# Performance work log

Measured on AMD Instinct MI355X. Metric: run time of the kernel, lower is better.

Reference implementation:

```python
import jax, jax.numpy as jnp
import numpy as np

# --- Config (Kimi/DeepSeek-style fine-grained MoE) ---
T = 4096        # num tokens
H = 1024        # hidden_size
I = 512         # moe_intermediate_size
E = 64          # num_experts
K = 8           # num_experts_per_token (top_k)
NG = 8          # num_expert_group
TKG = 4         # topk_group
NSH = 2         # num_shared_experts
IS = I * NSH    # shared-expert intermediate size
ROUTED_SCALE = 2.5


def setup_inputs() -> dict:
    key = jax.random.key(0)
    ks = jax.random.split(key, 7)
    s = 0.02
    return {
        "hidden_states": jax.random.normal(ks[0], (T, H), jnp.float32),
        "gate_w": jax.random.normal(ks[1], (E, H), jnp.float32) * s,          # router
        "e_bias": jax.random.normal(ks[2], (E,), jnp.float32) * 0.01,          # e_score_correction_bias
        "w1": jax.random.normal(ks[3], (E, H, 2 * I), jnp.float32) * s,       # per-expert gate_up
        "w2": jax.random.normal(ks[4], (E, I, H), jnp.float32) * s,           # per-expert down
        "sw_gu": jax.random.normal(ks[5], (H, 2 * IS), jnp.float32) * s,      # shared gate_up
        "sw_d": jax.random.normal(ks[6], (IS, H), jnp.float32) * s,           # shared down
    }


def _silu_and_mul(gu):
    d = gu.shape[-1] // 2
    return jax.nn.silu(gu[..., :d]) * gu[..., d:]


def _grouped_topk(scores, e_bias):
    """DeepSeek-V3/Kimi grouped top-k with sigmoid scoring + score-correction bias."""
    Tn = scores.shape[0]
    sfc = scores + e_bias[None, :]                       # scores_for_choice [T, E]
    # group score = sum of top-2 corrected scores inside each group
    grp = sfc.reshape(Tn, NG, E // NG)
    group_scores = jax.lax.top_k(grp, 2)[0].sum(-1)      # [T, NG]
    gidx = jax.lax.top_k(group_scores, TKG)[1]           # [T, TKG]
    gmask = jnp.zeros((Tn, NG), sfc.dtype).at[jnp.arange(Tn)[:, None], gidx].set(1.0)
    smask = jnp.repeat(gmask, E // NG, axis=1) > 0       # [T, E] bool
    tmp = jnp.where(smask, sfc, 0.0)                     # masked_fill(~mask, 0.0) as in vLLM
    topk_ids = jax.lax.top_k(tmp, K)[1]                  # [T, K]
    topk_w = jnp.take_along_axis(scores, topk_ids, axis=1)
    topk_w = topk_w / topk_w.sum(-1, keepdims=True)      # renormalize
    return topk_w, topk_ids


def _forward(x, gate_w, e_bias, w1, w2, sw_gu, sw_d):
    Tn, Hn = x.shape
    # shared experts (KimiMLP)
    shared = _silu_and_mul(x @ sw_gu) @ sw_d             # [T, H]
    # router
    logits = x @ gate_w.T                                # [T, E]
    scores = jax.nn.sigmoid(logits)
    topk_w, topk_ids = _grouped_topk(scores, e_bias)
    # dispatch: sort the T*K assignments by expert id -> grouped GEMM
    flat_ids = topk_ids.reshape(-1)                      # [T*K]
    order = jnp.argsort(flat_ids)                        # [T*K]
    tok = order // K                                     # token index of each sorted assignment
    xs = x[tok]                                          # [T*K, H] gathered tokens
    gsizes = jnp.bincount(flat_ids, length=E).astype(jnp.int32)
    gu = jax.lax.ragged_dot(xs, w1, gsizes)              # [T*K, 2I] grouped GEMM
    h = _silu_and_mul(gu)                                # [T*K, I]
    ys = jax.lax.ragged_dot(h, w2, gsizes)               # [T*K, H]
    # combine: scale by routing weight, scatter-add back to tokens
    flat_w = topk_w.reshape(-1)[order]                   # [T*K]
    routed = jnp.zeros((Tn, Hn), x.dtype).at[tok].add(ys * flat_w[:, None])
    return routed * ROUTED_SCALE + shared


def reference(hidden_states, gate_w, e_bias, w1, w2, sw_gu, sw_d):
    return _forward(hidden_states, gate_w, e_bias, w1, w2, sw_gu, sw_d)
```

## Files before the change

### kernel.cpp

```cpp
#include <hip/hip_runtime.h>
#include <cstdint>
#include <cstddef>

#define TT   4096
#define HH   1024
#define II   512
#define EE   64
#define KT   8
#define ISZ  1024
#define TKA  32768
#define MAXT 320

typedef __bf16 bf16x8 __attribute__((ext_vector_type(8)));
typedef float  f32x4  __attribute__((ext_vector_type(4)));
typedef unsigned short us8v __attribute__((ext_vector_type(8)));

__device__ __forceinline__ unsigned short f2bf(float f) {
  unsigned u = __float_as_uint(f);
  u += 0x7fffu + ((u >> 16) & 1u);
  return (unsigned short)(u >> 16);
}

#define GLDS(gp, lp) __builtin_amdgcn_global_load_lds( \
    (const __attribute__((address_space(1))) void*)(gp), \
    (__attribute__((address_space(3))) void*)(lp), 16, 0, 0)


__global__ __launch_bounds__(256) void k_transpose(const float* __restrict__ in,
                                                   unsigned short* __restrict__ out,
                                                   int R, int C) {
  __shared__ float tile[64][65];
  long b = blockIdx.z;
  int r0 = blockIdx.x * 64, c0 = blockIdx.y * 64;
  const float* ip = in + b * (long)R * C;
  unsigned short* op = out + b * (long)R * C;
  int tc = threadIdx.x & 63, tr = threadIdx.x >> 6;
#pragma unroll
  for (int rr = 0; rr < 64; rr += 4)
    tile[tr + rr][tc] = ip[(long)(r0 + tr + rr) * C + (c0 + tc)];
  __syncthreads();
#pragma unroll
  for (int rr = 0; rr < 64; rr += 4)
    op[(long)(c0 + tr + rr) * R + (r0 + tc)] = f2bf(tile[tc][tr + rr]);
}

__global__ __launch_bounds__(256) void k_cvt(const float* __restrict__ in,
                                             unsigned short* __restrict__ out) {
  int i = blockIdx.x * 256 + threadIdx.x;
  float4 v = ((const float4*)in)[i];
  ushort4 o;
  o.x = f2bf(v.x); o.y = f2bf(v.y); o.z = f2bf(v.z); o.w = f2bf(v.w);
  ((ushort4*)out)[i] = o;
}

__global__ __launch_bounds__(256) void k_router(const float* __restrict__ x,
    const float* __restrict__ gw, const float* __restrict__ eb,
    int* __restrict__ topk_ids, float* __restrict__ topk_w, int* __restrict__ counts)
{
  __shared__ float xrow[HH];
  __shared__ float sc[EE];
  int t = blockIdx.x;
  int tid = threadIdx.x;
  for (int i = tid; i < HH; i += 256) xrow[i] = x[(long)t * HH + i];
  __syncthreads();
  int e = tid >> 2, q = tid & 3;
  const float* w = gw + (long)e * HH;
  double acc = 0.0, acc2 = 0.0;
  for (int i = q * 8; i < HH; i += 32) {
    float4 wa = *(const float4*)(w + i);
    float4 wb = *(const float4*)(w + i + 4);
    acc  += (double)wa.x * (double)xrow[i]
          + (double)wa.y * (double)xrow[i + 1]
          + (double)wa.z * (double)xrow[i + 2]
          + (double)wa.w * (double)xrow[i + 3];
    acc2 += (double)wb.x * (double)xrow[i + 4]
          + (double)wb.y * (double)xrow[i + 5]
          + (double)wb.z * (double)xrow[i + 6]
          + (double)wb.w * (double)xrow[i + 7];
  }
  acc += acc2;
  acc += __shfl_down(acc, 2);
  acc += __shfl_down(acc, 1);
  if (q == 0) sc[e] = (float)(1.0 / (1.0 + exp(-acc)));
  __syncthreads();
  if (tid < 64) {
    int lane = tid;
    float s = sc[lane];
    float sfc = s + eb[lane];
    float m1 = sfc, m2 = -1e30f;
#pragma unroll
    for (int d = 1; d < 8; d <<= 1) {
      float o1 = __shfl_xor(m1, d);
      float o2 = __shfl_xor(m2, d);
      float hi = fmaxf(m1, o1);
      float lo = fminf(m1, o1);
      m2 = fmaxf(lo, fmaxf(m2, o2));
      m1 = hi;
    }
    float gs = m1 + m2;
    int g = lane >> 3;
    int grank = 0;
#pragma unroll
    for (int j = 0; j < 8; j++) {
      float gj = __shfl(gs, j * 8);
      if (gj > gs || (gj == gs && j < g)) grank++;
    }
    bool gsel = grank < 4;
    float mv = gsel ? sfc : 0.0f;
    int rank = 0;
    for (int j = 0; j < 64; j++) {
      float vj = __shfl(mv, j);
      if (vj > mv || (vj == mv && j < lane)) rank++;
    }
    bool sel = rank < KT;
    float ssum = sel ? s : 0.0f;
#pragma unroll
    for (int d = 1; d < 64; d <<= 1) ssum += __shfl_xor(ssum, d);
    unsigned long long bal = __ballot(sel);
    if (sel) {
      int pos = __popcll(bal & ((1ull << lane) - 1ull));
      topk_ids[(long)t * KT + pos] = lane;
      topk_w[(long)t * KT + pos] = s / ssum;
      atomicAdd(&counts[lane], 1);
    }
  }
}

__global__ void k_offsets(const int* __restrict__ counts, int* __restrict__ offsets,
                          int* __restrict__ cursor, int* __restrict__ tile_e,
                          int* __restrict__ tile_r0)
{
  int lane = threadIdx.x;
  int c = counts[lane];
  int xs = c;
#pragma unroll
  for (int d = 1; d < 64; d <<= 1) { int y = __shfl_up(xs, d); if (lane >= d) xs += y; }
  int off = xs - c;
  offsets[lane] = off;
  cursor[lane] = off;
  if (lane == 63) offsets[EE] = xs;
  int nt = (c + 127) >> 7;
  int tp = nt;
#pragma unroll
  for (int d = 1; d < 64; d <<= 1) { int y = __shfl_up(tp, d); if (lane >= d) tp += y; }
  int tbase = tp - nt;
  for (int i = 0; i < nt; i++) { tile_e[tbase + i] = lane; tile_r0[tbase + i] = off + i * 128; }
  int total = __shfl(tp, 63);
  for (int i = total + lane; i < MAXT; i += 64) tile_e[i] = -1;
}

__global__ __launch_bounds__(256) void k_scatter(const int* __restrict__ ids,
    const float* __restrict__ tw, int* __restrict__ cursor,
    int* __restrict__ perm, float* __restrict__ wslot, int* __restrict__ inv)
{
  int a = blockIdx.x * 256 + threadIdx.x;
  int e = ids[a];
  int pos = atomicAdd(&cursor[e], 1);
  perm[pos] = a >> 3;
  wslot[pos] = tw[a];
  inv[a] = pos;
}

__global__ __launch_bounds__(256) void k_gemm_gu(
    const unsigned short* __restrict__ Abase, const int* __restrict__ perm,
    const unsigned short* __restrict__ Bbase, long eStride, int Kd, int upOff,
    unsigned short* __restrict__ Hout,
    const int* __restrict__ tile_e, const int* __restrict__ tile_r0,
    const int* __restrict__ eoff, int rowsTotal)
{
  __shared__ __align__(16) unsigned short lds[24576];
  int e = 0, row0, end;
  if (tile_e) {
    e = tile_e[blockIdx.x];
    if (e < 0) return;
    row0 = tile_r0[blockIdx.x];
    end = eoff[e + 1];
  } else { row0 = blockIdx.x * 128; end = rowsTotal; }
  const unsigned short* B = Bbase + (long)e * eStride;
  int n0 = blockIdx.y * 64;
  int tid = threadIdx.x, lane = tid & 63, wave = tid >> 6;
  int wm = wave >> 1, wn = wave & 1;
  int lr = lane >> 2;
  int lkq = ((((lane & 3) - ((lane >> 3) & 3)) & 3)) * 8;
  int r0a = row0 + wave * 32 + lr;
  int r1a = r0a + 16;
  int t0 = r0a < rowsTotal ? r0a : rowsTotal - 1;
  int t1 = r1a < rowsTotal ? r1a : rowsTotal - 1;
  if (perm) { t0 = perm[t0]; t1 = perm[t1]; }
  const unsigned short* ap0 = Abase + (long)t0 * Kd + lkq;
  const unsigned short* ap1 = Abase + (long)t1 * Kd + lkq;
  const unsigned short* bg = B + (long)(n0 + wave * 16 + lr) * Kd + lkq;
  const unsigned short* bu = B + (long)(upOff + n0 + wave * 16 + lr) * Kd + lkq;
  unsigned short* lA0 = lds + wave * 1024 + lane * 8;
  unsigned short* lBg = lds + 4096 + wave * 512 + lane * 8;
  unsigned short* lBu = lds + 6144 + wave * 512 + lane * 8;
  f32x4 acc[4][4];
  f32x4 z = {0.f, 0.f, 0.f, 0.f};
  for (int i = 0; i < 4; i++) for (int j = 0; j < 4; j++) acc[i][j] = z;
  int quad = lane >> 4, cl = lane & 15;
  int sw8 = ((quad + ((cl >> 1) & 3)) & 3) * 8;
  int nk = Kd >> 5;
  GLDS(ap0, lA0);            GLDS(ap1, lA0 + 512);
  GLDS(bg,  lBg);            GLDS(bu,  lBu);
  GLDS(ap0 + 32, lA0 + 8192); GLDS(ap1 + 32, lA0 + 8192 + 512);
  GLDS(bg + 32,  lBg + 8192); GLDS(bu + 32,  lBu + 8192);
  int cur = 0, nxt = 8192, fut = 16384;
  for (int t = 0; t < nk; ++t) {
    __builtin_amdgcn_s_barrier();
    if (t + 2 < nk) {
      int k2 = (t + 2) << 5;
      GLDS(ap0 + k2, lA0 + fut); GLDS(ap1 + k2, lA0 + fut + 512);
      GLDS(bg + k2,  lBg + fut); GLDS(bu + k2,  lBu + fut);
      asm volatile("s_waitcnt vmcnt(8)" ::: "memory");
    } else if (t + 1 < nk) {
      asm volatile("s_waitcnt vmcnt(4)" ::: "memory");
    } else {
      asm volatile("s_waitcnt vmcnt(0)" ::: "memory");
    }
    __builtin_amdgcn_s_barrier();
    asm volatile("" ::: "memory");
    bf16x8 af[4], bgf[2], buf2[2];
#pragma unroll
    for (int mi = 0; mi < 4; mi++)
      af[mi] = *(const bf16x8*)(lds + cur + (wm * 64 + mi * 16 + cl) * 32 + sw8);
#pragma unroll
    for (int ni = 0; ni < 2; ni++) {
      bgf[ni]  = *(const bf16x8*)(lds + cur + 4096 + (wn * 32 + ni * 16 + cl) * 32 + sw8);
      buf2[ni] = *(const bf16x8*)(lds + cur + 6144 + (wn * 32 + ni * 16 + cl) * 32 + sw8);
    }
#pragma unroll
    for (int mi = 0; mi < 4; mi++) {
#pragma unroll
      for (int ni = 0; ni < 2; ni++) {
        acc[mi][ni]     = __builtin_amdgcn_mfma_f32_16x16x32_bf16(af[mi], bgf[ni],  acc[mi][ni],     0, 0, 0);
        acc[mi][ni + 2] = __builtin_amdgcn_mfma_f32_16x16x32_bf16(af[mi], buf2[ni], acc[mi][ni + 2], 0, 0, 0);
      }
    }
    asm volatile("" ::: "memory");
    int tmp = cur; cur = nxt; nxt = fut; fut = tmp;
  }
#pragma unroll
  for (int mi = 0; mi < 4; mi++) {
#pragma unroll
    for (int j = 0; j < 2; j++) {
#pragma unroll
      for (int r = 0; r < 4; r++) {
        int row = row0 + wm * 64 + mi * 16 + quad * 4 + r;
        if (row < end) {
          float g = acc[mi][j][r], u = acc[mi][j + 2][r];
          float hv = g * (1.f / (1.f + __expf(-g))) * u;
          Hout[(long)row * upOff + (n0 + wn * 32 + j * 16 + cl)] = f2bf(hv);
        }
      }
    }
  }
}

__global__ __launch_bounds__(256) void k_gemm_down(
    const unsigned short* __restrict__ Abase,
    const unsigned short* __restrict__ Bbase, long eStride, int Kd,
    void* __restrict__ Outv, const float* __restrict__ wslot,
    const int* __restrict__ tile_e, const int* __restrict__ tile_r0,
    const int* __restrict__ eoff, int rowsTotal, int mode)
{
  __shared__ __align__(16) unsigned short lds[24576];
  int e = 0, row0, end;
  if (tile_e) {
    e = tile_e[blockIdx.x];
    if (e < 0) return;
    row0 = tile_r0[blockIdx.x];
    end = eoff[e + 1];
  } else { row0 = blockIdx.x * 128; end = rowsTotal; }
  const unsigned short* B = Bbase + (long)e * eStride;
  int n0 = blockIdx.y * 128;
  int tid = threadIdx.x, lane = tid & 63, wave = tid >> 6;
  int wm = wave >> 1, wn = wave & 1;
  int lr = lane >> 2;
  int lkq = ((((lane & 3) - ((lane >> 3) & 3)) & 3)) * 8;
  int r0a = row0 + wave * 32 + lr;
  int r1a = r0a + 16;
  int t0 = r0a < rowsTotal ? r0a : rowsTotal - 1;
  int t1 = r1a < rowsTotal ? r1a : rowsTotal - 1;
  const unsigned short* ap0 = Abase + (long)t0 * Kd + lkq;
  const unsigned short* ap1 = Abase + (long)t1 * Kd + lkq;
  const unsigned short* bp0 = B + (long)(n0 + wave * 32 + lr) * Kd + lkq;
  const unsigned short* bp1 = bp0 + (long)16 * Kd;
  unsigned short* lA0 = lds + wave * 1024 + lane * 8;
  unsigned short* lB0 = lds + 4096 + wave * 1024 + lane * 8;
  f32x4 acc[4][4];
  f32x4 z = {0.f, 0.f, 0.f, 0.f};
  for (int i = 0; i < 4; i++) for (int j = 0; j < 4; j++) acc[i][j] = z;
  int quad = lane >> 4, cl = lane & 15;
  int sw8 = ((quad + ((cl >> 1) & 3)) & 3) * 8;
  int nk = Kd >> 5;
  GLDS(ap0, lA0);             GLDS(ap1, lA0 + 512);
  GLDS(bp0, lB0);             GLDS(bp1, lB0 + 512);
  GLDS(ap0 + 32, lA0 + 8192); GLDS(ap1 + 32, lA0 + 8192 + 512);
  GLDS(bp0 + 32, lB0 + 8192); GLDS(bp1 + 32, lB0 + 8192 + 512);
  int cur = 0, nxt = 8192, fut = 16384;
  for (int t = 0; t < nk; ++t) {
    __builtin_amdgcn_s_barrier();
    if (t + 2 < nk) {
      int k2 = (t + 2) << 5;
      GLDS(ap0 + k2, lA0 + fut); GLDS(ap1 + k2, lA0 + fut + 512);
      GLDS(bp0 + k2, lB0 + fut); GLDS(bp1 + k2, lB0 + fut + 512);
      asm volatile("s_waitcnt vmcnt(8)" ::: "memory");
    } else if (t + 1 < nk) {
      asm volatile("s_waitcnt vmcnt(4)" ::: "memory");
    } else {
      asm volatile("s_waitcnt vmcnt(0)" ::: "memory");
    }
    __builtin_amdgcn_s_barrier();
    asm volatile("" ::: "memory");
    bf16x8 af[4], bfr[4];
#pragma unroll
    for (int mi = 0; mi < 4; mi++)
      af[mi] = *(const bf16x8*)(lds + cur + (wm * 64 + mi * 16 + cl) * 32 + sw8);
#pragma unroll
    for (int ni = 0; ni < 4; ni++)
      bfr[ni] = *(const bf16x8*)(lds + cur + 4096 + (wn * 64 + ni * 16 + cl) * 32 + sw8);
#pragma unroll
    for (int mi = 0; mi < 4; mi++)
#pragma unroll
      for (int ni = 0; ni < 4; ni++)
        acc[mi][ni] = __builtin_amdgcn_mfma_f32_16x16x32_bf16(af[mi], bfr[ni], acc[mi][ni], 0, 0, 0);
    asm volatile("" ::: "memory");
    int tmp = cur; cur = nxt; nxt = fut; fut = tmp;
  }
#pragma unroll
  for (int mi = 0; mi < 4; mi++) {
    int rowb = row0 + wm * 64 + mi * 16 + quad * 4;
#pragma unroll
    for (int r = 0; r < 4; r++) {
      int row = rowb + r;
      if (row >= end) continue;
      if (mode) {
        unsigned short* Y = (unsigned short*)Outv;
        float scale = wslot[row] * 2.5f;
#pragma unroll
        for (int ni = 0; ni < 4; ni++) {
          int col = n0 + wn * 64 + ni * 16 + cl;
          Y[(long)row * HH + col] = f2bf(acc[mi][ni][r] * scale);
        }
      } else {
        float* O = (float*)Outv;
#pragma unroll
        for (int ni = 0; ni < 4; ni++) {
          int col = n0 + wn * 64 + ni * 16 + cl;
          O[(long)row * HH + col] = acc[mi][ni][r];
        }
      }
    }
  }
}

__global__ __launch_bounds__(256) void k_combine(const unsigned short* __restrict__ ys,
    const int* __restrict__ inv, float* __restrict__ out)
{
  int idx = blockIdx.x * 256 + threadIdx.x;
  int t = idx >> 7, c0 = (idx & 127) << 3;
  const int* ip = inv + (long)t * KT;
  float* op = out + (long)t * HH + c0;
  float4 o0 = *(float4*)op;
  float4 o1 = *(float4*)(op + 4);
  float a[8] = {o0.x, o0.y, o0.z, o0.w, o1.x, o1.y, o1.z, o1.w};
#pragma unroll
  for (int k = 0; k < KT; k++) {
    us8v v = *(const us8v*)(ys + (long)ip[k] * HH + c0);
#pragma unroll
    for (int j = 0; j < 8; j++) a[j] += __uint_as_float((unsigned)v[j] << 16);
  }
  *(float4*)op = make_float4(a[0], a[1], a[2], a[3]);
  *(float4*)(op + 4) = make_float4(a[4], a[5], a[6], a[7]);
}

extern "C" void kernel_launch(void* const* d_in, const int* in_sizes, int n_in,
                              void* d_out, int out_size, void* d_ws, size_t ws_size,
                              hipStream_t stream)
{
  const float* x   = (const float*)d_in[0];
  const float* gw  = (const float*)d_in[1];
  const float* eb  = (const float*)d_in[2];
  const float* w1  = (const float*)d_in[3];
  const float* w2  = (const float*)d_in[4];
  const float* sgu = (const float*)d_in[5];
  const float* sd  = (const float*)d_in[6];
  float* out = (float*)d_out;
  char* ws = (char*)d_ws;
  size_t off = 0;
  auto alloc = [&](size_t b) { void* p = ws + off; off += (b + 255) & ~(size_t)255; return p; };
  unsigned short* w1t  = (unsigned short*)alloc((size_t)EE * 2 * II * HH * 2);
  unsigned short* w2t  = (unsigned short*)alloc((size_t)EE * HH * II * 2);
  unsigned short* sgut = (unsigned short*)alloc((size_t)2 * ISZ * HH * 2);
  unsigned short* sdt  = (unsigned short*)alloc((size_t)HH * ISZ * 2);
  unsigned short* xb   = (unsigned short*)alloc((size_t)TT * HH * 2);
  unsigned short* hsb  = (unsigned short*)alloc((size_t)TT * ISZ * 2);
  unsigned short* hb   = (unsigned short*)alloc((size_t)TKA * II * 2);
  unsigned short* ys   = (unsigned short*)alloc((size_t)TKA * HH * 2);
  int*   tids   = (int*)alloc((size_t)TKA * 4);
  float* tw     = (float*)alloc((size_t)TKA * 4);
  int*   counts = (int*)alloc(256);
  int*   offs   = (int*)alloc(512);
  int*   cursor = (int*)alloc(256);
  int*   tile_e = (int*)alloc(MAXT * 4);
  int*   tile_r = (int*)alloc(MAXT * 4);
  int*   perm   = (int*)alloc((size_t)TKA * 4);
  float* wslot  = (float*)alloc((size_t)TKA * 4);
  int*   inv    = (int*)alloc((size_t)TKA * 4);

  hipMemsetAsync(counts, 0, 256, stream);
  dim3 b256(256);
  k_transpose<<<dim3(HH / 64, (2 * II) / 64, EE), b256, 0, stream>>>(w1, w1t, HH, 2 * II);
  k_transpose<<<dim3(II / 64, HH / 64, EE), b256, 0, stream>>>(w2, w2t, II, HH);
  k_transpose<<<dim3(HH / 64, (2 * ISZ) / 64, 1), b256, 0, stream>>>(sgu, sgut, HH, 2 * ISZ);
  k_transpose<<<dim3(ISZ / 64, HH / 64, 1), b256, 0, stream>>>(sd, sdt, ISZ, HH);
  k_cvt<<<dim3((TT * HH) / 1024), b256, 0, stream>>>(x, xb);
  k_router<<<dim3(TT), b256, 0, stream>>>(x, gw, eb, tids, tw, counts);
  k_offsets<<<dim3(1), dim3(64), 0, stream>>>(counts, offs, cursor, tile_e, tile_r);
  k_scatter<<<dim3(TKA / 256), b256, 0, stream>>>(tids, tw, cursor, perm, wslot, inv);
  k_gemm_gu<<<dim3(MAXT, II / 64), b256, 0, stream>>>(xb, perm, w1t, (long)2 * II * HH, HH, II,
                                                      hb, tile_e, tile_r, offs, TKA);
  k_gemm_down<<<dim3(MAXT, HH / 128), b256, 0, stream>>>(hb, w2t, (long)HH * II, II, (void*)ys,
                                                         wslot, tile_e, tile_r, offs, TKA, 1);
  k_gemm_gu<<<dim3(TT / 128, ISZ / 64), b256, 0, stream>>>(xb, nullptr, sgut, 0, HH, ISZ,
                                                           hsb, nullptr, nullptr, nullptr, TT);
  k_gemm_down<<<dim3(TT / 128, HH / 128), b256, 0, stream>>>(hsb, sdt, 0, ISZ, (void*)out,
                                                             nullptr, nullptr, nullptr, nullptr, TT, 0);
  k_combine<<<dim3(TT * 128 / 256), b256, 0, stream>>>(ys, inv, out);
}
```

Before: 942.2 us.

## Pre-tile weights and intermediates into MFMA-swizzled blocks; remap GEMM grid for L2 locality

Weight transposes now write bf16 data in 16-row by 32-k blocks with the LDS swizzle already applied. Each wave's global-to-LDS load then reads one contiguous 1KB chunk instead of strided rows. Each expert's row range is padded to a multiple of 16 so the gate/up GEMM can write its activation output in the same tiled layout for the down GEMM. Both GEMMs also remap block IDs into 8 chunks to group tiles for cache reuse. This adds padding buffers, zero-fill work in the offsets kernel, and more complex index math.

```diff
diff --git a/kernel.cpp b/kernel.cpp
--- a/kernel.cpp
+++ b/kernel.cpp
@@ -9,6 +9,7 @@
 #define KT   8
 #define ISZ  1024
 #define TKA  32768
+#define TKAP (TKA + 2048)
 #define MAXT 320
 
 typedef __bf16 bf16x8 __attribute__((ext_vector_type(8)));
@@ -39,9 +40,20 @@
   for (int rr = 0; rr < 64; rr += 4)
     tile[tr + rr][tc] = ip[(long)(r0 + tr + rr) * C + (c0 + tc)];
   __syncthreads();
-#pragma unroll
-  for (int rr = 0; rr < 64; rr += 4)
-    op[(long)(c0 + tr + rr) * R + (r0 + tc)] = f2bf(tile[tc][tr + rr]);
+  int kt = R >> 5;
+#pragma unroll
+  for (int p = 0; p < 2; p++) {
+    int sid = p * 256 + threadIdx.x;
+    int nl = sid >> 3, kq = sid & 7;
+    int n = c0 + nl;
+    int kg = r0 + kq * 8;
+    int s = ((kq & 3) + ((n >> 1) & 3)) & 3;
+    long off = ((long)(n >> 4) * kt + (kg >> 5)) * 512 + (n & 15) * 32 + s * 8;
+    us8v v;
+#pragma unroll
+    for (int j = 0; j < 8; j++) v[j] = f2bf(tile[kq * 8 + j][nl]);
+    *(us8v*)(op + off) = v;
+  }
 }
 
 __global__ __launch_bounds__(256) void k_cvt(const float* __restrict__ in,
@@ -128,14 +140,16 @@
 
 __global__ void k_offsets(const int* __restrict__ counts, int* __restrict__ offsets,
                           int* __restrict__ cursor, int* __restrict__ tile_e,
-                          int* __restrict__ tile_r0)
+                          int* __restrict__ tile_r0, int* __restrict__ perm,
+                          float* __restrict__ wslot)
 {
   int lane = threadIdx.x;
   int c = counts[lane];
-  int xs = c;
+  int ca = (c + 15) & ~15;
+  int xs = ca;
 #pragma unroll
   for (int d = 1; d < 64; d <<= 1) { int y = __shfl_up(xs, d); if (lane >= d) xs += y; }
-  int off = xs - c;
+  int off = xs - ca;
   offsets[lane] = off;
   cursor[lane] = off;
   if (lane == 63) offsets[EE] = xs;
@@ -147,6 +161,10 @@
   for (int i = 0; i < nt; i++) { tile_e[tbase + i] = lane; tile_r0[tbase + i] = off + i * 128; }
   int total = __shfl(tp, 63);
   for (int i = total + lane; i < MAXT; i += 64) tile_e[i] = -1;
+  for (int i = off + c; i < off + ca; i++) { perm[i] = 0; wslot[i] = 0.f; }
+  int ptotal = __shfl(xs, 63);
+  int lastEnd = __shfl(off + nt * 128, 63);
+  for (int i = ptotal + lane; i < lastEnd; i += 64) { perm[i] = 0; wslot[i] = 0.f; }
 }
 
 __global__ __launch_bounds__(256) void k_scatter(const int* __restrict__ ids,
@@ -169,15 +187,20 @@
     const int* __restrict__ eoff, int rowsTotal)
 {
   __shared__ __align__(16) unsigned short lds[24576];
+  int D = blockIdx.y * gridDim.x + blockIdx.x;
+  int cx = D & 7, jj = D >> 3;
+  int chunk = gridDim.x >> 3;
+  int mt = cx * chunk + jj / gridDim.y;
+  int ny = jj - (jj / gridDim.y) * gridDim.y;
   int e = 0, row0, end;
   if (tile_e) {
-    e = tile_e[blockIdx.x];
+    e = tile_e[mt];
     if (e < 0) return;
-    row0 = tile_r0[blockIdx.x];
+    row0 = tile_r0[mt];
     end = eoff[e + 1];
-  } else { row0 = blockIdx.x * 128; end = rowsTotal; }
+  } else { row0 = mt * 128; end = rowsTotal; }
   const unsigned short* B = Bbase + (long)e * eStride;
-  int n0 = blockIdx.y * 64;
+  int n0 = ny * 64;
   int tid = threadIdx.x, lane = tid & 63, wave = tid >> 6;
   int wm = wave >> 1, wn = wave & 1;
   int lr = lane >> 2;
@@ -189,8 +212,12 @@
   if (perm) { t0 = perm[t0]; t1 = perm[t1]; }
   const unsigned short* ap0 = Abase + (long)t0 * Kd + lkq;
   const unsigned short* ap1 = Abase + (long)t1 * Kd + lkq;
-  const unsigned short* bg = B + (long)(n0 + wave * 16 + lr) * Kd + lkq;
-  const unsigned short* bu = B + (long)(upOff + n0 + wave * 16 + lr) * Kd + lkq;
+  int nkt = Kd >> 5;
+  const unsigned short* bgp = Bbase + (long)e * eStride
+      + ((long)((n0 >> 4) + wave) * nkt) * 512 + lane * 8;
+  const unsigned short* bup = Bbase + (long)e * eStride
+      + ((long)(((upOff + n0) >> 4) + wave) * nkt) * 512 + lane * 8;
+  (void)B;
   unsigned short* lA0 = lds + wave * 1024 + lane * 8;
   unsigned short* lBg = lds + 4096 + wave * 512 + lane * 8;
   unsigned short* lBu = lds + 6144 + wave * 512 + lane * 8;
@@ -200,17 +227,18 @@
   int quad = lane >> 4, cl = lane & 15;
   int sw8 = ((quad + ((cl >> 1) & 3)) & 3) * 8;
   int nk = Kd >> 5;
-  GLDS(ap0, lA0);            GLDS(ap1, lA0 + 512);
-  GLDS(bg,  lBg);            GLDS(bu,  lBu);
+  GLDS(ap0, lA0);             GLDS(ap1, lA0 + 512);
+  GLDS(bgp, lBg);             GLDS(bup, lBu);
   GLDS(ap0 + 32, lA0 + 8192); GLDS(ap1 + 32, lA0 + 8192 + 512);
-  GLDS(bg + 32,  lBg + 8192); GLDS(bu + 32,  lBu + 8192);
+  GLDS(bgp + 512, lBg + 8192); GLDS(bup + 512, lBu + 8192);
   int cur = 0, nxt = 8192, fut = 16384;
   for (int t = 0; t < nk; ++t) {
     __builtin_amdgcn_s_barrier();
     if (t + 2 < nk) {
       int k2 = (t + 2) << 5;
       GLDS(ap0 + k2, lA0 + fut); GLDS(ap1 + k2, lA0 + fut + 512);
-      GLDS(bg + k2,  lBg + fut); GLDS(bu + k2,  lBu + fut);
+      GLDS(bgp + (long)(t + 2) * 512, lBg + fut);
+      GLDS(bup + (long)(t + 2) * 512, lBu + fut);
       asm volatile("s_waitcnt vmcnt(8)" ::: "memory");
     } else if (t + 1 < nk) {
       asm volatile("s_waitcnt vmcnt(4)" ::: "memory");
@@ -239,6 +267,7 @@
     asm volatile("" ::: "memory");
     int tmp = cur; cur = nxt; nxt = fut; fut = tmp;
   }
+  int ntO = upOff >> 5;
 #pragma unroll
   for (int mi = 0; mi < 4; mi++) {
 #pragma unroll
@@ -249,7 +278,11 @@
         if (row < end) {
           float g = acc[mi][j][r], u = acc[mi][j + 2][r];
           float hv = g * (1.f / (1.f + __expf(-g))) * u;
-          Hout[(long)row * upOff + (n0 + wn * 32 + j * 16 + cl)] = f2bf(hv);
+          int col = n0 + wn * 32 + j * 16 + cl;
+          int sl = (((col >> 3) & 3) + ((row >> 1) & 3)) & 3;
+          long offp = ((long)(row >> 4) * ntO + (col >> 5)) * 512
+                    + (row & 15) * 32 + sl * 8 + (col & 7);
+          Hout[offp] = f2bf(hv);
         }
       }
     }
@@ -264,27 +297,27 @@
     const int* __restrict__ eoff, int rowsTotal, int mode)
 {
   __shared__ __align__(16) unsigned short lds[24576];
+  int D = blockIdx.y * gridDim.x + blockIdx.x;
+  int cx = D & 7, jj = D >> 3;
+  int chunk = gridDim.x >> 3;
+  int mt = cx * chunk + jj / gridDim.y;
+  int ny = jj - (jj / gridDim.y) * gridDim.y;
   int e = 0, row0, end;
   if (tile_e) {
-    e = tile_e[blockIdx.x];
+    e = tile_e[mt];
     if (e < 0) return;
-    row0 = tile_r0[blockIdx.x];
+    row0 = tile_r0[mt];
     end = eoff[e + 1];
-  } else { row0 = blockIdx.x * 128; end = rowsTotal; }
-  const unsigned short* B = Bbase + (long)e * eStride;
-  int n0 = blockIdx.y * 128;
+  } else { row0 = mt * 128; end = rowsTotal; }
+  int n0 = ny * 128;
   int tid = threadIdx.x, lane = tid & 63, wave = tid >> 6;
   int wm = wave >> 1, wn = wave & 1;
-  int lr = lane >> 2;
-  int lkq = ((((lane & 3) - ((lane >> 3) & 3)) & 3)) * 8;
-  int r0a = row0 + wave * 32 + lr;
-  int r1a = r0a + 16;
-  int t0 = r0a < rowsTotal ? r0a : rowsTotal - 1;
-  int t1 = r1a < rowsTotal ? r1a : rowsTotal - 1;
-  const unsigned short* ap0 = Abase + (long)t0 * Kd + lkq;
-  const unsigned short* ap1 = Abase + (long)t1 * Kd + lkq;
-  const unsigned short* bp0 = B + (long)(n0 + wave * 32 + lr) * Kd + lkq;
-  const unsigned short* bp1 = bp0 + (long)16 * Kd;
+  int nkt = Kd >> 5;
+  long sstep = (long)nkt * 512;
+  const unsigned short* apk = Abase
+      + ((long)((row0 >> 4) + 2 * wave) * nkt) * 512 + lane * 8;
+  const unsigned short* bpk = Bbase + (long)e * eStride
+      + ((long)((n0 >> 4) + 2 * wave) * nkt) * 512 + lane * 8;
   unsigned short* lA0 = lds + wave * 1024 + lane * 8;
   unsigned short* lB0 = lds + 4096 + wave * 1024 + lane * 8;
   f32x4 acc[4][4];
@@ -293,17 +326,17 @@
   int quad = lane >> 4, cl = lane & 15;
   int sw8 = ((quad + ((cl >> 1) & 3)) & 3) * 8;
   int nk = Kd >> 5;
-  GLDS(ap0, lA0);             GLDS(ap1, lA0 + 512);
-  GLDS(bp0, lB0);             GLDS(bp1, lB0 + 512);
-  GLDS(ap0 + 32, lA0 + 8192); GLDS(ap1 + 32, lA0 + 8192 + 512);
-  GLDS(bp0 + 32, lB0 + 8192); GLDS(bp1 + 32, lB0 + 8192 + 512);
+  GLDS(apk, lA0);              GLDS(apk + sstep, lA0 + 512);
+  GLDS(bpk, lB0);              GLDS(bpk + sstep, lB0 + 512);
+  GLDS(apk + 512, lA0 + 8192); GLDS(apk + sstep + 512, lA0 + 8192 + 512);
+  GLDS(bpk + 512, lB0 + 8192); GLDS(bpk + sstep + 512, lB0 + 8192 + 512);
   int cur = 0, nxt = 8192, fut = 16384;
   for (int t = 0; t < nk; ++t) {
     __builtin_amdgcn_s_barrier();
     if (t + 2 < nk) {
-      int k2 = (t + 2) << 5;
-      GLDS(ap0 + k2, lA0 + fut); GLDS(ap1 + k2, lA0 + fut + 512);
-      GLDS(bp0 + k2, lB0 + fut); GLDS(bp1 + k2, lB0 + fut + 512);
+      long k2 = (long)(t + 2) * 512;
+      GLDS(apk + k2, lA0 + fut); GLDS(apk + sstep + k2, lA0 + fut + 512);
+      GLDS(bpk + k2, lB0 + fut); GLDS(bpk + sstep + k2, lB0 + fut + 512);
       asm volatile("s_waitcnt vmcnt(8)" ::: "memory");
     } else if (t + 1 < nk) {
       asm volatile("s_waitcnt vmcnt(4)" ::: "memory");
@@ -395,8 +428,8 @@
   unsigned short* sdt  = (unsigned short*)alloc((size_t)HH * ISZ * 2);
   unsigned short* xb   = (unsigned short*)alloc((size_t)TT * HH * 2);
   unsigned short* hsb  = (unsigned short*)alloc((size_t)TT * ISZ * 2);
-  unsigned short* hb   = (unsigned short*)alloc((size_t)TKA * II * 2);
-  unsigned short* ys   = (unsigned short*)alloc((size_t)TKA * HH * 2);
+  unsigned short* hb   = (unsigned short*)alloc((size_t)TKAP * II * 2);
+  unsigned short* ys   = (unsigned short*)alloc((size_t)TKAP * HH * 2);
   int*   tids   = (int*)alloc((size_t)TKA * 4);
   float* tw     = (float*)alloc((size_t)TKA * 4);
   int*   counts = (int*)alloc(256);
@@ -404,8 +437,8 @@
   int*   cursor = (int*)alloc(256);
   int*   tile_e = (int*)alloc(MAXT * 4);
   int*   tile_r = (int*)alloc(MAXT * 4);
-  int*   perm   = (int*)alloc((size_t)TKA * 4);
-  float* wslot  = (float*)alloc((size_t)TKA * 4);
+  int*   perm   = (int*)alloc((size_t)TKAP * 4);
+  float* wslot  = (float*)alloc((size_t)TKAP * 4);
   int*   inv    = (int*)alloc((size_t)TKA * 4);
 
   hipMemsetAsync(counts, 0, 256, stream);
@@ -416,12 +449,12 @@
   k_transpose<<<dim3(ISZ / 64, HH / 64, 1), b256, 0, stream>>>(sd, sdt, ISZ, HH);
   k_cvt<<<dim3((TT * HH) / 1024), b256, 0, stream>>>(x, xb);
   k_router<<<dim3(TT), b256, 0, stream>>>(x, gw, eb, tids, tw, counts);
-  k_offsets<<<dim3(1), dim3(64), 0, stream>>>(counts, offs, cursor, tile_e, tile_r);
+  k_offsets<<<dim3(1), dim3(64), 0, stream>>>(counts, offs, cursor, tile_e, tile_r, perm, wslot);
   k_scatter<<<dim3(TKA / 256), b256, 0, stream>>>(tids, tw, cursor, perm, wslot, inv);
   k_gemm_gu<<<dim3(MAXT, II / 64), b256, 0, stream>>>(xb, perm, w1t, (long)2 * II * HH, HH, II,
-                                                      hb, tile_e, tile_r, offs, TKA);
+                                                      hb, tile_e, tile_r, offs, TKAP);
   k_gemm_down<<<dim3(MAXT, HH / 128), b256, 0, stream>>>(hb, w2t, (long)HH * II, II, (void*)ys,
-                                                         wslot, tile_e, tile_r, offs, TKA, 1);
+                                                         wslot, tile_e, tile_r, offs, TKAP, 1);
   k_gemm_gu<<<dim3(TT / 128, ISZ / 64), b256, 0, stream>>>(xb, nullptr, sgut, 0, HH, ISZ,
                                                            hsb, nullptr, nullptr, nullptr, TT);
   k_gemm_down<<<dim3(TT / 128, HH / 128), b256, 0, stream>>>(hsb, sdt, 0, ISZ, (void*)out,
```

New measurement: 859.4 us. -8.8%, faster.
